# Optimization experiments

Measured on AMD Instinct MI355X. Metric: run time of the kernel, lower is better.

The kernel has to match this reference:

```python
import jax, jax.numpy as jnp
from jax import lax
import numpy as np

P = 7            # patch_size
NP = 10          # n_patches
WIN = 20         # window_size
STRIDE = 4       # window loop stride
EMB = 128        # embedding_dimension
L = WIN - P + 1  # valid-conv output side (14)
HALF = WIN // 2 - P // 2  # window start offset before clipping (7)


def _positions(H, W):
    # x outer, y inner, exactly matching the nested python loops in the source
    return np.array([(x, y) for x in range(0, H - WIN + 1, STRIDE)
                     for y in range(0, W - WIN + 1, STRIDE)], dtype=np.int32)


def _forward(images, Wp, bp, pos_emb, Wb, bb):
    B, C, H, W = images.shape
    BC = B * C
    pos = jnp.asarray(_positions(H, W))  # [Ppos, 2]

    def per_pos(p):
        x, y = p[0], p[1]
        xb0 = jnp.maximum(x - HALF, 0)          # clipped window start (x / cols)
        yb0 = jnp.maximum(y - HALF, 0)          # clipped window start (y / rows)
        winW = jnp.minimum(x - HALF + WIN, W) - xb0  # clipped window width
        winH = jnp.minimum(y - HALF + WIN, H) - yb0  # clipped window height
        # reference patch: rows y:y+P, cols x:x+P (from ORIGINAL data, as in source)
        ref = lax.dynamic_slice(images, (0, 0, y, x), (B, C, P, P)).reshape(BC, 1, P, P)
        # fixed-size window slice; upper bound never clips for our dims, lower-clip
        # handled by masking invalid candidate offsets below
        win = lax.dynamic_slice(images, (0, 0, yb0, xb0), (B, C, WIN, WIN)).reshape(BC, WIN, WIN)
        # grouped cross-correlation == torch conv2d(groups=BC) similarity
        sim = lax.conv_general_dilated(win[None], ref, (1, 1), 'VALID',
                                       feature_group_count=BC,
                                       dimension_numbers=('NCHW', 'OIHW', 'NCHW'))[0]  # [BC,L,L]
        valid = (jnp.arange(L)[:, None] <= winH - P) & (jnp.arange(L)[None, :] <= winW - P)
        sim = jnp.where(valid[None], sim, -jnp.inf)
        _, idx = lax.top_k(sim.reshape(BC, L * L), NP)  # [BC, NP]
        oy, ox = idx // L, idx % L  # row / col offsets inside the window

        def extract(w2, a, b):
            # source's meshgrid indexing yields the TRANSPOSED patch, flattened
            return lax.dynamic_slice(w2, (a, b), (P, P)).T.reshape(P * P)
        patches = jax.vmap(jax.vmap(extract, in_axes=(None, 0, 0)))(win, oy, ox)  # [BC,NP,P*P]
        # source bug kept: x_coords = row offset + x window start (and vice versa)
        return patches, oy + xb0, ox + yb0

    patches, xi, yi = jax.vmap(per_pos)(pos)  # [Ppos,BC,NP,49], [Ppos,BC,NP] int32 x2

    # NOTE: the TransformerEncoder output is discarded in the source; the actual
    # math is back_projection(projection(patches) + pos_emb).
    emb = patches.reshape(-1, B, C, NP, P * P) @ Wp + bp + pos_emb  # [Ppos,B,C,NP,EMB]
    den = (emb @ Wb + bb).reshape(-1, BC, NP, P, P)                 # [Ppos,BC,NP,P,P]

    img0 = images.reshape(BC, H, W)
    cnt0 = jnp.ones((BC, H, W), images.dtype)

    def upd(im, cn, x_i, y_i, d):
        reg = lax.dynamic_slice(im, (y_i, x_i), (P, P))
        c = lax.dynamic_slice(cn, (y_i, x_i), (P, P))
        im = lax.dynamic_update_slice(im, (reg * c + d) / (c + 1.0), (y_i, x_i))
        # source bug kept: counter incremented at transposed slice [x, y]
        ct = lax.dynamic_slice(cn, (x_i, y_i), (P, P)) + 1.0
        cn = lax.dynamic_update_slice(cn, ct, (x_i, y_i))
        return im, cn
    vupd = jax.vmap(upd)  # (b,c) planes are independent -> vectorize

    def n_step(carry, t):
        d, x_i, y_i = t
        return vupd(carry[0], carry[1], x_i, y_i, d), None

    def pos_step(carry, t):
        d, x_i, y_i = t  # d:[BC,NP,P,P]
        carry, _ = lax.scan(n_step, carry, (jnp.moveaxis(d, 1, 0), x_i.T, y_i.T))
        return carry, None

    (img, _), _ = lax.scan(pos_step, (img0, cnt0), (den, xi, yi))
    return img.reshape(B, C, H, W)


def setup_inputs() -> dict:
    key = jax.random.key(0)
    k0, k1, k2, k3 = jax.random.split(key, 4)
    B, C, H, W = 4, 8, 160, 160
    return {
        'images': jax.random.normal(k0, (B, C, H, W), jnp.float32),
        'Wp': jax.random.normal(k1, (P * P, EMB), jnp.float32) * 0.05,
        'bp': jnp.zeros((EMB,), jnp.float32),
        'pos_emb': jax.random.normal(k2, (1, NP, EMB), jnp.float32),
        'Wb': jax.random.normal(k3, (EMB, P * P), jnp.float32) * 0.05,
        'bb': jnp.zeros((P * P,), jnp.float32),
    }


def reference(images, Wp, bp, pos_emb, Wb, bb):
    return _forward(images, Wp, bp, pos_emb, Wb, bb)
```

## Files before the change

### kernel.cpp

```cpp
#include <hip/hip_runtime.h>

#define PS 7
#define NP 10
#define WIN 20
#define STR 4
#define LL 14
#define HALF 7
#define HH 160
#define WW 160
#define BCN 32
#define NX 36
#define PPOS 1296
#define EMBD 128
#define NTASK (BCN * PPOS * NP)
#define NEV (PPOS * NP)
#define CAP 512
#define NTILE 400

__global__ __launch_bounds__(256) void k_mk(const float* __restrict__ Wp,
                                            const float* __restrict__ bp,
                                            const float* __restrict__ pe,
                                            const float* __restrict__ Wb,
                                            const float* __restrict__ bb,
                                            float* __restrict__ M,
                                            float* __restrict__ K) {
    int t = blockIdx.x * 256 + threadIdx.x;
    if (t < 49 * 49) {
        int k = t / 49, d = t % 49;
        float acc = 0.f;
        for (int e = 0; e < EMBD; ++e) acc += Wp[k * EMBD + e] * Wb[e * 49 + d];
        M[t] = acc;
    } else if (t < 49 * 49 + NP * 49) {
        int u = t - 49 * 49;
        int n = u / 49, d = u % 49;
        float acc = bb[d];
        for (int e = 0; e < EMBD; ++e) acc += (bp[e] + pe[n * EMBD + e]) * Wb[e * 49 + d];
        K[u] = acc;
    }
}

__global__ __launch_bounds__(64) void k_sim(const float* __restrict__ img,
                                            unsigned* __restrict__ xy,
                                            float* __restrict__ pd) {
    int blk = blockIdx.x;
    int pos = blk % PPOS;
    int bc  = blk / PPOS;
    int lane = threadIdx.x;
    int ix = pos / NX, iy = pos % NX;
    int x = ix * STR, y = iy * STR;
    int xb0 = max(x - HALF, 0), yb0 = max(y - HALF, 0);
    int jmax = x + 6 - xb0;
    int imax = y + 6 - yb0;
    const float* plane = img + bc * (HH * WW);

    float v[4];
#pragma unroll
    for (int s = 0; s < 4; ++s) {
        int q = lane + s * 64;
        float acc = -INFINITY;
        if (q < 196) {
            int i = q / 14, j = q % 14;
            const float* wbase = plane + (yb0 + i) * WW + (xb0 + j);
            float a2 = 0.f;
#pragma unroll
            for (int a = 0; a < PS; ++a)
#pragma unroll
                for (int b = 0; b < PS; ++b)
                    a2 += wbase[a * WW + b] * plane[(y + a) * WW + (x + b)];
            acc = (i > imax || j > jmax) ? -INFINITY : a2;
        }
        v[s] = acc;
    }

    int a_ = lane / 7, b_ = lane % 7;
    int voffE = b_ * WW + a_;
    bool act = lane < 49;
    int tbase = (bc * PPOS + pos) * NP;

    for (int n = 0; n < NP; ++n) {
        float bv = fmaxf(fmaxf(v[0], v[1]), fmaxf(v[2], v[3]));
#pragma unroll
        for (int off = 32; off >= 1; off >>= 1)
            bv = fmaxf(bv, __shfl_xor(bv, off));
        unsigned long long m0 = __ballot(v[0] == bv);
        unsigned long long m1 = __ballot(v[1] == bv);
        unsigned long long m2 = __ballot(v[2] == bv);
        unsigned long long m3 = __ballot(v[3] == bv);
        int s_w = m0 ? 0 : (m1 ? 1 : (m2 ? 2 : 3));
        unsigned long long mw = m0 ? m0 : (m1 ? m1 : (m2 ? m2 : m3));
        int w  = __ffsll(mw) - 1;
        int bi = s_w * 64 + w;
#pragma unroll
        for (int s = 0; s < 4; ++s)
            if (s == s_w && lane == w) v[s] = -INFINITY;

        int oy = bi / 14, ox = bi % 14;
        int x_i = oy + xb0;
        int y_i = ox + yb0;
        int t = tbase + n;
        if (lane == 0) xy[t] = (unsigned)x_i | ((unsigned)y_i << 8);
        const float* src = plane + (yb0 + oy) * WW + (xb0 + ox);
        if (act) pd[(size_t)t * 49 + lane] = src[voffE];
    }
}

__global__ __launch_bounds__(256) void k_den(float* __restrict__ pd,
                                             const float* __restrict__ Mg,
                                             const float* __restrict__ Kg) {
    __shared__ float Ps[256 * 49];
    int tid = threadIdx.x;
    size_t base = (size_t)blockIdx.x * (256 * 49);
    for (int i = tid; i < 256 * 49; i += 256) Ps[i] = pd[base + i];
    __syncthreads();

    int t = blockIdx.x * 256 + tid;
    int n = t % NP;
    float acc[49];
#pragma unroll
    for (int d = 0; d < 49; ++d) acc[d] = Kg[n * 49 + d];
    for (int k = 0; k < 49; ++k) {
        float p = Ps[tid * 49 + k];
        const float* mrow = Mg + k * 49;
#pragma unroll
        for (int d = 0; d < 49; ++d) acc[d] += p * mrow[d];
    }
    __syncthreads();
#pragma unroll
    for (int d = 0; d < 49; ++d) Ps[tid * 49 + d] = acc[d];
    __syncthreads();
    for (int i = tid; i < 256 * 49; i += 256) pd[base + i] = Ps[i];
}

__global__ __launch_bounds__(256) void k_apply(const float* __restrict__ img,
                                               const unsigned* __restrict__ xy,
                                               const float* __restrict__ pd,
                                               float* __restrict__ out) {
    __shared__ unsigned lsts[4][CAP];
    int tid  = threadIdx.x;
    int wv   = tid >> 6;
    int lane = tid & 63;
    int gt   = blockIdx.x * 4 + wv;
    int bc   = gt / NTILE;
    int tile = gt % NTILE;
    int tx0 = (tile % 20) * 8, ty0 = (tile / 20) * 8;
    int tx1 = tx0 + 7, ty1 = ty0 + 7;
    const unsigned* xs = xy + bc * NEV;
    unsigned* lst = lsts[wv];

    int a0 = (tx0 <= 19) ? 0 : ((tx0 - 9) >> 2), a1 = min(35, (tx0 + 14) >> 2);
    int b0 = (ty0 <= 19) ? 0 : ((ty0 - 9) >> 2), b1 = min(35, (ty0 + 14) >> 2);
    if (a0 > b0) { int t0 = a0; a0 = b0; b0 = t0; int t1 = a1; a1 = b1; b1 = t1; }
    int lo0 = a0, lo1 = 0, len0, len1;
    if (b0 <= a1 + 1) { len0 = max(a1, b1) - lo0 + 1; len1 = 0; }
    else              { len0 = a1 - a0 + 1; lo1 = b0; len1 = b1 - b0 + 1; }
    int nU = len0 + len1;
    unsigned m = 65536u / (unsigned)nU + 1u;
    int npos = nU * nU;

    unsigned cnt = 0;
    for (int base = 0; base < npos; base += 64) {
        int k = base + lane;
        bool valid = k < npos;
        unsigned kk = valid ? (unsigned)k : 0u;
        int ki = (int)((kk * m) >> 16);
        int kj = (int)kk - ki * nU;
        int ixp = (ki < len0) ? (lo0 + ki) : (lo1 + ki - len0);
        int iyp = (kj < len0) ? (lo0 + kj) : (lo1 + kj - len0);
        int pos = ixp * NX + iyp;
        const unsigned* ep = xs + pos * NP;

        unsigned ev[NP];
#pragma unroll
        for (int n = 0; n < NP; ++n) ev[n] = ep[n];

        unsigned rel = 0;
        unsigned pk[NP];
#pragma unroll
        for (int n = 0; n < NP; ++n) {
            unsigned u = ev[n];
            int x_i = (int)(u & 255u);
            int y_i = (int)((u >> 8) & 255u);
            bool ih = (x_i <= tx1) && (x_i + 6 >= tx0) &&
                      (y_i <= ty1) && (y_i + 6 >= ty0);
            bool ch = (x_i <= ty1) && (x_i + 6 >= ty0) &&
                      (y_i <= tx1) && (y_i + 6 >= tx0);
            bool any = valid && (ih || ch);
            rel |= any ? (1u << n) : 0u;
            pk[n] = (unsigned)(pos * NP + n) | ((unsigned)x_i << 14) | ((unsigned)y_i << 22)
                  | (ih ? (1u << 30) : 0u) | (ch ? (1u << 31) : 0u);
        }
        int myc = __popc(rel);
        int scan = myc;
#pragma unroll
        for (int off = 1; off < 64; off <<= 1) {
            int o = __shfl_up(scan, off);
            scan += (lane >= off) ? o : 0;
        }
        int excl  = (int)cnt + scan - myc;
        int total = __shfl(scan, 63);
        int w = excl;
#pragma unroll
        for (int n = 0; n < NP; ++n) {
            if ((rel >> n) & 1u) { if (w < CAP) lst[w] = pk[n]; ++w; }
        }
        cnt += (unsigned)total;
    }
    if (cnt > CAP) cnt = CAP;
    unsigned cntp = (cnt + 7u) & ~7u;
    if (cntp > CAP) cntp = CAP;
    if (lane < (int)(cntp - cnt)) lst[cnt + lane] = 0u;
    int cntN = (int)cntp;

    int r  = ty0 + (lane >> 3);
    int cc = tx0 + (lane & 7);
    float im = img[bc * (HH * WW) + r * WW + cc];
    float c  = 1.0f;
    const float* ds = pd + (size_t)bc * ((size_t)NEV * 49);
    int vOff = (r * 7 + cc) * 4;

    for (int i = 0; i < cntN; i += 8) {
        unsigned eu[8];
        float    dv[8];
#pragma unroll
        for (int j = 0; j < 8; ++j)
            eu[j] = (unsigned)__builtin_amdgcn_readfirstlane((int)lst[i + j]);
#pragma unroll
        for (int j = 0; j < 8; ++j) {
            unsigned u = eu[j];
            int t    = (int)(u & 16383u);
            int x_i  = (int)((u >> 14) & 255u);
            int y_i  = (int)((u >> 22) & 255u);
            int sOff = (y_i * 7 + x_i) * 4;
            const char* dsb = (const char*)(ds + (size_t)t * 49);
            int boc = min(max(vOff - sOff, 0), 192);
            dv[j] = *(const float*)(dsb + boc);
        }
#pragma unroll
        for (int j = 0; j < 8; ++j) {
            unsigned u = eu[j];
            int x_i = (int)((u >> 14) & 255u);
            int y_i = (int)((u >> 22) & 255u);
            int dr = r - y_i, dc = cc - x_i;
            bool h = (u & (1u << 30)) && (((unsigned)dr <= 6u) & ((unsigned)dc <= 6u));
            float nim = fmaf(im, c, dv[j]) * __builtin_amdgcn_rcpf(c + 1.0f);
            im = h ? nim : im;
            int er = r - x_i, ec = cc - y_i;
            bool hc = (u >> 31) && (((unsigned)er <= 6u) & ((unsigned)ec <= 6u));
            c += hc ? 1.0f : 0.0f;
        }
    }
    out[bc * (HH * WW) + r * WW + cc] = im;
}

extern "C" void kernel_launch(void* const* d_in, const int* in_sizes, int n_in,
                              void* d_out, int out_size, void* d_ws, size_t ws_size,
                              hipStream_t stream) {
    const float* img = (const float*)d_in[0];
    const float* Wp  = (const float*)d_in[1];
    const float* bp  = (const float*)d_in[2];
    const float* pe  = (const float*)d_in[3];
    const float* Wb  = (const float*)d_in[4];
    const float* bb  = (const float*)d_in[5];
    float* out = (float*)d_out;

    float* wsf = (float*)d_ws;
    float*    M   = wsf;
    float*    K   = wsf + 2404;
    unsigned* xy  = (unsigned*)(wsf + 2896);
    float*    pd  = wsf + 2896 + NTASK;

    k_mk<<<12, 256, 0, stream>>>(Wp, bp, pe, Wb, bb, M, K);
    k_sim<<<BCN * PPOS, 64, 0, stream>>>(img, xy, pd);
    k_den<<<NTASK / 256, 256, 0, stream>>>(pd, M, K);
    k_apply<<<BCN * NTILE / 4, 256, 0, stream>>>(img, xy, pd, out);
}
```

Measured before the change: 352.3 us.

## Stage similarity windows in LDS and drop shared-memory staging in denoise kernel

k_sim now runs four positions per 256-thread block. Each wave loads its 20x20 window into LDS, and both the correlation and the patch extraction read from that copy instead of repeatedly reading global memory. k_den drops its 49KB shared-memory staging and loads each thread's 49-float row straight into registers, then writes the results back directly. This raises occupancy for k_den, but its per-thread strided global accesses are uncoalesced and register pressure goes up.

Measured after the change: 605.7 us. +71.9%, slower.

```diff
diff --git a/kernel.cpp b/kernel.cpp
--- a/kernel.cpp
+++ b/kernel.cpp
@@ -39,19 +39,32 @@
     }
 }
 
-__global__ __launch_bounds__(64) void k_sim(const float* __restrict__ img,
-                                            unsigned* __restrict__ xy,
-                                            float* __restrict__ pd) {
-    int blk = blockIdx.x;
-    int pos = blk % PPOS;
-    int bc  = blk / PPOS;
-    int lane = threadIdx.x;
+__global__ __launch_bounds__(256) void k_sim(const float* __restrict__ img,
+                                             unsigned* __restrict__ xy,
+                                             float* __restrict__ pd) {
+    __shared__ float winS[4][400];
+    int tid  = threadIdx.x;
+    int wv   = tid >> 6;
+    int lane = tid & 63;
+    int gt   = blockIdx.x * 4 + wv;
+    int pos  = gt % PPOS;
+    int bc   = gt / PPOS;
     int ix = pos / NX, iy = pos % NX;
     int x = ix * STR, y = iy * STR;
     int xb0 = max(x - HALF, 0), yb0 = max(y - HALF, 0);
     int jmax = x + 6 - xb0;
     int imax = y + 6 - yb0;
     const float* plane = img + bc * (HH * WW);
+    float* win = winS[wv];
+
+#pragma unroll
+    for (int it = 0; it < 7; ++it) {
+        int idx = lane + it * 64;
+        if (idx < 400) {
+            int rr = idx / 20, cc2 = idx % 20;
+            win[idx] = plane[(yb0 + rr) * WW + xb0 + cc2];
+        }
+    }
 
     float v[4];
 #pragma unroll
@@ -60,20 +73,20 @@
         float acc = -INFINITY;
         if (q < 196) {
             int i = q / 14, j = q % 14;
-            const float* wbase = plane + (yb0 + i) * WW + (xb0 + j);
+            const float* wbase = &win[i * 20 + j];
             float a2 = 0.f;
 #pragma unroll
             for (int a = 0; a < PS; ++a)
 #pragma unroll
                 for (int b = 0; b < PS; ++b)
-                    a2 += wbase[a * WW + b] * plane[(y + a) * WW + (x + b)];
+                    a2 += wbase[a * 20 + b] * plane[(y + a) * WW + (x + b)];
             acc = (i > imax || j > jmax) ? -INFINITY : a2;
         }
         v[s] = acc;
     }
 
     int a_ = lane / 7, b_ = lane % 7;
-    int voffE = b_ * WW + a_;
+    int voffL = b_ * 20 + a_;
     bool act = lane < 49;
     int tbase = (bc * PPOS + pos) * NP;
 
@@ -99,36 +112,30 @@
         int y_i = ox + yb0;
         int t = tbase + n;
         if (lane == 0) xy[t] = (unsigned)x_i | ((unsigned)y_i << 8);
-        const float* src = plane + (yb0 + oy) * WW + (xb0 + ox);
-        if (act) pd[(size_t)t * 49 + lane] = src[voffE];
+        if (act) pd[(size_t)t * 49 + lane] = win[oy * 20 + ox + voffL];
     }
 }
 
 __global__ __launch_bounds__(256) void k_den(float* __restrict__ pd,
                                              const float* __restrict__ Mg,
                                              const float* __restrict__ Kg) {
-    __shared__ float Ps[256 * 49];
-    int tid = threadIdx.x;
-    size_t base = (size_t)blockIdx.x * (256 * 49);
-    for (int i = tid; i < 256 * 49; i += 256) Ps[i] = pd[base + i];
-    __syncthreads();
-
-    int t = blockIdx.x * 256 + tid;
+    int t = blockIdx.x * 256 + threadIdx.x;
     int n = t % NP;
+    float* row = pd + (size_t)t * 49;
+    float p[49];
+#pragma unroll
+    for (int k = 0; k < 49; ++k) p[k] = row[k];
     float acc[49];
 #pragma unroll
     for (int d = 0; d < 49; ++d) acc[d] = Kg[n * 49 + d];
     for (int k = 0; k < 49; ++k) {
-        float p = Ps[tid * 49 + k];
+        float pk = p[k];
         const float* mrow = Mg + k * 49;
 #pragma unroll
-        for (int d = 0; d < 49; ++d) acc[d] += p * mrow[d];
-    }
-    __syncthreads();
-#pragma unroll
-    for (int d = 0; d < 49; ++d) Ps[tid * 49 + d] = acc[d];
-    __syncthreads();
-    for (int i = tid; i < 256 * 49; i += 256) pd[base + i] = Ps[i];
+        for (int d = 0; d < 49; ++d) acc[d] += pk * mrow[d];
+    }
+#pragma unroll
+    for (int d = 0; d < 49; ++d) row[d] = acc[d];
 }
 
 __global__ __launch_bounds__(256) void k_apply(const float* __restrict__ img,
@@ -270,7 +277,7 @@
     float*    pd  = wsf + 2896 + NTASK;
 
     k_mk<<<12, 256, 0, stream>>>(Wp, bp, pe, Wb, bb, M, K);
-    k_sim<<<BCN * PPOS, 64, 0, stream>>>(img, xy, pd);
+    k_sim<<<BCN * PPOS / 4, 256, 0, stream>>>(img, xy, pd);
     k_den<<<NTASK / 256, 256, 0, stream>>>(pd, M, K);
     k_apply<<<BCN * NTILE / 4, 256, 0, stream>>>(img, xy, pd, out);
 }
```
